# Optimization experiments

Hardware: AMD Instinct MI355X
Metric: run time of the kernel (lower is better)

## Reference

```python
import jax, jax.numpy as jnp
import numpy as np

TWO_PI = 2.0 * np.pi

def ringify(x):
    # wrap values to [-pi, pi)
    return (x + np.pi) % TWO_PI - np.pi

def complex_mean(x, axes):
    # circular mean direction: atan2(sum sin, sum ringify(cos))
    dir_x = ringify(jnp.cos(x)).sum(axis=axes)
    dir_y = jnp.sin(x).sum(axis=axes)
    return jnp.arctan2(dir_y, dir_x)

def setup_inputs() -> dict:
    key = jax.random.key(0)
    k1, k2, k3, k4 = jax.random.split(key, 4)
    B = 4096
    return {
        "x": jax.random.normal(k1, (B, 1, 28, 28), dtype=jnp.float32),
        "conv1_w": jax.random.normal(k2, (4, 1, 2, 2), dtype=jnp.float32),
        "conv2_w": jax.random.normal(k3, (8, 4, 4, 4), dtype=jnp.float32),
        "ff_w": jax.random.normal(k4, (288, 10), dtype=jnp.float32),
    }

def reference(x, conv1_w, conv2_w, ff_w):
    B = x.shape[0]
    x = ringify(x).reshape(B, 1, 28, 28)

    # --- ring conv1: 2x2 kernel, stride 2 (non-overlapping patches) ---
    # [B,1,28,28] -> [B,14,14,1,2,2]  (matches unfold(2,2,2).unfold(3,2,2).permute)
    p1 = x.reshape(B, 1, 14, 2, 14, 2).transpose(0, 2, 4, 1, 3, 5)
    w1 = conv1_w.transpose(1, 2, 3, 0)            # [1,2,2,4]
    d1 = ringify(p1[..., None] - w1)              # [B,14,14,1,2,2,4]
    h1 = complex_mean(d1, (3, 4, 5))              # [B,14,14,4]

    # --- ring conv2: 4x4 kernel, stride 2 (overlapping patches) ---
    h1 = h1.transpose(0, 3, 1, 2)                 # [B,4,14,14]
    idx = (jnp.arange(6) * 2)[:, None] + jnp.arange(4)[None, :]  # [6,4] window rows/cols
    p2 = h1[:, :, idx, :][:, :, :, :, idx]        # [B,4,6,4,6,4]
    p2 = p2.transpose(0, 2, 4, 1, 3, 5)           # [B,6,6,4,4,4]
    w2 = conv2_w.transpose(1, 2, 3, 0)            # [4,4,4,8]
    d2 = ringify(p2[..., None] - w2)              # [B,6,6,4,4,4,8]
    h2 = complex_mean(d2, (3, 4, 5))              # [B,6,6,8]

    # --- ring feed-forward ---
    f = h2.reshape(B, 288)
    d3 = ringify(f[:, :, None] - ff_w)            # [B,288,10]
    out = complex_mean(d3, (1,))                  # [B,10]
    return jnp.sin(out)
```

## Files before the change

### kernel.cpp

```cpp
#include <hip/hip_runtime.h>
#include <math.h>

#define W1_OFF 0
#define W2_OFF 16
#define NTRIG_SM 528
#define NFF 2880

__global__ void precompute_ff(const float* __restrict__ ff, float2* __restrict__ out) {
    int i = blockIdx.x * blockDim.x + threadIdx.x;
    if (i < NFF) {
        float s, c; sincosf(ff[i], &s, &c);
        out[i] = make_float2(c, s);
    }
}

template <bool USE_WS>
__global__ __launch_bounds__(640) void ringnn_kernel(
    const float* __restrict__ x,
    const float* __restrict__ w1g,
    const float* __restrict__ w2g,
    const float* __restrict__ ffg,
    const float2* __restrict__ fft_ws,
    float* __restrict__ out)
{
    __shared__ float2 trig[NTRIG_SM];
    __shared__ float2 sc1[2 * 784];
    __shared__ float2 sc2[2 * 288];
    __shared__ float2 ff_lds[USE_WS ? 1 : NFF];

    const int tid = threadIdx.x;

    if (tid < 16) {
        float s, c; __sincosf(w1g[tid], &s, &c);
        trig[W1_OFF + tid] = make_float2(c, s);
    }
    {
        int i = tid - 64;
        if (i >= 0 && i < 512) {
            int oc = i >> 6, e = i & 63;
            float s, c; __sincosf(w2g[i], &s, &c);
            trig[W2_OFF + e * 8 + oc] = make_float2(c, s);
        }
    }
    if (!USE_WS) {
        for (int i = tid; i < NFF; i += 640) {
            float s, c; __sincosf(ffg[i], &s, &c);
            ff_lds[i] = make_float2(c, s);
        }
    }
    __syncthreads();

    if (tid < 392) {
        int img = tid / 196, pos = tid % 196;
        int i = pos / 14, j = pos % 14;
        const float* xb = x + ((size_t)blockIdx.x * 2 + img) * 784;
        float2 r0 = *(const float2*)(xb + (2 * i) * 28 + 2 * j);
        float2 r1 = *(const float2*)(xb + (2 * i + 1) * 28 + 2 * j);
        float sx[4], cx[4];
        __sincosf(r0.x, &sx[0], &cx[0]);
        __sincosf(r0.y, &sx[1], &cx[1]);
        __sincosf(r1.x, &sx[2], &cx[2]);
        __sincosf(r1.y, &sx[3], &cx[3]);
        #pragma unroll
        for (int oc = 0; oc < 4; oc++) {
            float Y = 0.f, X = 0.f;
            #pragma unroll
            for (int e = 0; e < 4; e++) {
                float2 w = trig[W1_OFF + oc * 4 + e];
                Y = fmaf(sx[e], w.x, fmaf(-cx[e], w.y, Y));
                X = fmaf(cx[e], w.x, fmaf( sx[e], w.y, X));
            }
            float inv = rsqrtf(fmaxf(fmaf(X, X, Y * Y), 1e-30f));
            sc1[img * 784 + oc * 196 + pos] = make_float2(Y * inv, X * inv);
        }
    }
    __syncthreads();

    if (tid < 576) {
        int img = tid / 288;
        int r = tid % 288;
        int p = r >> 3, q = r & 7;
        int ocp = q >> 1, hf = q & 1;
        int oi = p / 6, oj = p % 6;
        const float2* scb = sc1 + img * 784;
        int base = oi * 28 + oj * 2;
        float Y0 = 0.f, X0 = 0.f, Y1 = 0.f, X1 = 0.f;
        #pragma unroll
        for (int ch = 0; ch < 4; ch++) {
            #pragma unroll
            for (int kk = 0; kk < 2; kk++) {
                int ki = hf * 2 + kk;
                #pragma unroll
                for (int jp = 0; jp < 2; jp++) {
                    int kj = jp * 2;
                    float4 sp = *(const float4*)(scb + ch * 196 + base + ki * 14 + kj);
                    int e = ch * 16 + ki * 4 + kj;
                    float4 w0 = *(const float4*)(&trig[W2_OFF + e * 8 + ocp * 2]);
                    float4 w1 = *(const float4*)(&trig[W2_OFF + (e + 1) * 8 + ocp * 2]);
                    Y0 = fmaf(sp.x, w0.x, fmaf(-sp.y, w0.y, Y0));
                    X0 = fmaf(sp.y, w0.x, fmaf( sp.x, w0.y, X0));
                    Y1 = fmaf(sp.x, w0.z, fmaf(-sp.y, w0.w, Y1));
                    X1 = fmaf(sp.y, w0.z, fmaf( sp.x, w0.w, X1));
                    Y0 = fmaf(sp.z, w1.x, fmaf(-sp.w, w1.y, Y0));
                    X0 = fmaf(sp.w, w1.x, fmaf( sp.z, w1.y, X0));
                    Y1 = fmaf(sp.z, w1.z, fmaf(-sp.w, w1.w, Y1));
                    X1 = fmaf(sp.w, w1.z, fmaf( sp.z, w1.w, X1));
                }
            }
        }
        Y0 += __shfl_xor(Y0, 1); X0 += __shfl_xor(X0, 1);
        Y1 += __shfl_xor(Y1, 1); X1 += __shfl_xor(X1, 1);
        float Y = hf ? Y1 : Y0;
        float X = hf ? X1 : X0;
        float inv = rsqrtf(fmaxf(fmaf(X, X, Y * Y), 1e-30f));
        sc2[img * 288 + p * 8 + ocp * 2 + hf] = make_float2(Y * inv, X * inv);
    }
    __syncthreads();

    {
        int img = tid / 320;
        int r = tid % 320;
        int n = r >> 5, s = r & 31;
        const float2* scb = sc2 + img * 288;
        float Y = 0.f, X = 0.f;
        #pragma unroll
        for (int i = 0; i < 9; i++) {
            int k = s * 9 + i;
            float2 sc = scb[k];
            float2 w;
            if (USE_WS) w = fft_ws[k * 10 + n];
            else        w = ff_lds[k * 10 + n];
            Y = fmaf(sc.x, w.x, fmaf(-sc.y, w.y, Y));
            X = fmaf(sc.y, w.x, fmaf( sc.x, w.y, X));
        }
        #pragma unroll
        for (int off = 16; off > 0; off >>= 1) {
            Y += __shfl_down(Y, off, 32);
            X += __shfl_down(X, off, 32);
        }
        if (s == 0) {
            size_t b = (size_t)blockIdx.x * 2 + img;
            out[b * 10 + n] = Y * rsqrtf(fmaxf(fmaf(X, X, Y * Y), 1e-30f));
        }
    }
}

extern "C" void kernel_launch(void* const* d_in, const int* in_sizes, int n_in,
                              void* d_out, int out_size, void* d_ws, size_t ws_size,
                              hipStream_t stream) {
    const float* x  = (const float*)d_in[0];
    const float* w1 = (const float*)d_in[1];
    const float* w2 = (const float*)d_in[2];
    const float* ff = (const float*)d_in[3];
    float* out = (float*)d_out;
    const int B = in_sizes[0] / 784;

    if (ws_size >= NFF * sizeof(float2)) {
        float2* fft = (float2*)d_ws;
        precompute_ff<<<(NFF + 255) / 256, 256, 0, stream>>>(ff, fft);
        ringnn_kernel<true><<<B / 2, 640, 0, stream>>>(x, w1, w2, ff, fft, out);
    } else {
        ringnn_kernel<false><<<B / 2, 640, 0, stream>>>(x, w1, w2, ff, nullptr, out);
    }
}
```

Baseline: 93.07 us.

## Drop ff precompute kernel, register-tile conv2, pad sc1 layout, recompute ff trig inline

Removes the separate ff precompute launch and workspace path. The feed-forward stage now computes sincos of the ff weights inline from global memory, with 16 lanes per output instead of 32. Conv2 is register-tiled so each thread computes three output columns and reuses loaded patches across kj, with only 192 threads active. The sc1 layout is padded to rows of 18, and the conv2 weights are regrouped per output-channel pair to allow wide LDS loads. This trades one fewer launch and less LDS traffic for redundant transcendental work in the FF stage and lower thread utilisation in conv2.

```diff
diff --git a/kernel.cpp b/kernel.cpp
--- a/kernel.cpp
+++ b/kernel.cpp
@@ -1,59 +1,36 @@
 #include <hip/hip_runtime.h>
 #include <math.h>
 
-#define W1_OFF 0
-#define W2_OFF 16
-#define NTRIG_SM 528
-#define NFF 2880
+#define B_PER_BLK 2
 
-__global__ void precompute_ff(const float* __restrict__ ff, float2* __restrict__ out) {
-    int i = blockIdx.x * blockDim.x + threadIdx.x;
-    if (i < NFF) {
-        float s, c; sincosf(ff[i], &s, &c);
-        out[i] = make_float2(c, s);
-    }
-}
-
-template <bool USE_WS>
 __global__ __launch_bounds__(640) void ringnn_kernel(
     const float* __restrict__ x,
     const float* __restrict__ w1g,
     const float* __restrict__ w2g,
     const float* __restrict__ ffg,
-    const float2* __restrict__ fft_ws,
     float* __restrict__ out)
 {
-    __shared__ float2 trig[NTRIG_SM];
-    __shared__ float2 sc1[2 * 784];
-    __shared__ float2 sc2[2 * 288];
-    __shared__ float2 ff_lds[USE_WS ? 1 : NFF];
-
+    __shared__ float2 trig1[16];
+    __shared__ float2 trig2[520];
+    __shared__ float2 sc1[B_PER_BLK * 1008];
+    __shared__ float2 sc2[B_PER_BLK * 288];
     const int tid = threadIdx.x;
 
     if (tid < 16) {
         float s, c; __sincosf(w1g[tid], &s, &c);
-        trig[W1_OFF + tid] = make_float2(c, s);
+        trig1[tid] = make_float2(c, s);
     }
-    {
-        int i = tid - 64;
-        if (i >= 0 && i < 512) {
-            int oc = i >> 6, e = i & 63;
-            float s, c; __sincosf(w2g[i], &s, &c);
-            trig[W2_OFF + e * 8 + oc] = make_float2(c, s);
-        }
-    }
-    if (!USE_WS) {
-        for (int i = tid; i < NFF; i += 640) {
-            float s, c; __sincosf(ffg[i], &s, &c);
-            ff_lds[i] = make_float2(c, s);
-        }
+    if (tid < 512) {
+        int oc = tid >> 6, e = tid & 63;
+        float s, c; __sincosf(w2g[tid], &s, &c);
+        trig2[(oc >> 1) * 130 + e * 2 + (oc & 1)] = make_float2(c, s);
     }
     __syncthreads();
 
     if (tid < 392) {
         int img = tid / 196, pos = tid % 196;
         int i = pos / 14, j = pos % 14;
-        const float* xb = x + ((size_t)blockIdx.x * 2 + img) * 784;
+        const float* xb = x + ((size_t)blockIdx.x * B_PER_BLK + img) * 784;
         float2 r0 = *(const float2*)(xb + (2 * i) * 28 + 2 * j);
         float2 r1 = *(const float2*)(xb + (2 * i + 1) * 28 + 2 * j);
         float sx[4], cx[4];
@@ -63,83 +40,93 @@
         __sincosf(r1.y, &sx[3], &cx[3]);
         #pragma unroll
         for (int oc = 0; oc < 4; oc++) {
+            float4 wa = *(const float4*)(&trig1[oc * 4]);
+            float4 wb = *(const float4*)(&trig1[oc * 4 + 2]);
             float Y = 0.f, X = 0.f;
-            #pragma unroll
-            for (int e = 0; e < 4; e++) {
-                float2 w = trig[W1_OFF + oc * 4 + e];
-                Y = fmaf(sx[e], w.x, fmaf(-cx[e], w.y, Y));
-                X = fmaf(cx[e], w.x, fmaf( sx[e], w.y, X));
-            }
+            Y = fmaf(sx[0], wa.x, fmaf(-cx[0], wa.y, Y));
+            X = fmaf(cx[0], wa.x, fmaf( sx[0], wa.y, X));
+            Y = fmaf(sx[1], wa.z, fmaf(-cx[1], wa.w, Y));
+            X = fmaf(cx[1], wa.z, fmaf( sx[1], wa.w, X));
+            Y = fmaf(sx[2], wb.x, fmaf(-cx[2], wb.y, Y));
+            X = fmaf(cx[2], wb.x, fmaf( sx[2], wb.y, X));
+            Y = fmaf(sx[3], wb.z, fmaf(-cx[3], wb.w, Y));
+            X = fmaf(cx[3], wb.z, fmaf( sx[3], wb.w, X));
             float inv = rsqrtf(fmaxf(fmaf(X, X, Y * Y), 1e-30f));
-            sc1[img * 784 + oc * 196 + pos] = make_float2(Y * inv, X * inv);
+            sc1[img * 1008 + oc * 252 + i * 18 + j] = make_float2(Y * inv, X * inv);
         }
     }
     __syncthreads();
 
-    if (tid < 576) {
-        int img = tid / 288;
-        int r = tid % 288;
-        int p = r >> 3, q = r & 7;
-        int ocp = q >> 1, hf = q & 1;
-        int oi = p / 6, oj = p % 6;
-        const float2* scb = sc1 + img * 784;
-        int base = oi * 28 + oj * 2;
-        float Y0 = 0.f, X0 = 0.f, Y1 = 0.f, X1 = 0.f;
+    if (tid < 192) {
+        int img = tid / 96, r = tid % 96;
+        int oi = r >> 4, ojg = (r >> 3) & 1, ocp = (r >> 1) & 3, hf = r & 1;
+        const float2* scb = sc1 + img * 1008;
+        const float2* wbp = trig2 + ocp * 130;
+        float aY[3][2] = {{0.f,0.f},{0.f,0.f},{0.f,0.f}};
+        float aX[3][2] = {{0.f,0.f},{0.f,0.f},{0.f,0.f}};
         #pragma unroll
         for (int ch = 0; ch < 4; ch++) {
             #pragma unroll
             for (int kk = 0; kk < 2; kk++) {
                 int ki = hf * 2 + kk;
+                int base = ch * 252 + (oi * 2 + ki) * 18 + ojg * 6;
+                float4 f0 = *(const float4*)(scb + base);
+                float4 f1 = *(const float4*)(scb + base + 2);
+                float4 f2 = *(const float4*)(scb + base + 4);
+                float4 f3 = *(const float4*)(scb + base + 6);
+                float ss[8] = {f0.x,f0.z,f1.x,f1.z,f2.x,f2.z,f3.x,f3.z};
+                float cc[8] = {f0.y,f0.w,f1.y,f1.w,f2.y,f2.w,f3.y,f3.w};
+                int e0 = ch * 16 + ki * 4;
                 #pragma unroll
-                for (int jp = 0; jp < 2; jp++) {
-                    int kj = jp * 2;
-                    float4 sp = *(const float4*)(scb + ch * 196 + base + ki * 14 + kj);
-                    int e = ch * 16 + ki * 4 + kj;
-                    float4 w0 = *(const float4*)(&trig[W2_OFF + e * 8 + ocp * 2]);
-                    float4 w1 = *(const float4*)(&trig[W2_OFF + (e + 1) * 8 + ocp * 2]);
-                    Y0 = fmaf(sp.x, w0.x, fmaf(-sp.y, w0.y, Y0));
-                    X0 = fmaf(sp.y, w0.x, fmaf( sp.x, w0.y, X0));
-                    Y1 = fmaf(sp.x, w0.z, fmaf(-sp.y, w0.w, Y1));
-                    X1 = fmaf(sp.y, w0.z, fmaf( sp.x, w0.w, X1));
-                    Y0 = fmaf(sp.z, w1.x, fmaf(-sp.w, w1.y, Y0));
-                    X0 = fmaf(sp.w, w1.x, fmaf( sp.z, w1.y, X0));
-                    Y1 = fmaf(sp.z, w1.z, fmaf(-sp.w, w1.w, Y1));
-                    X1 = fmaf(sp.w, w1.z, fmaf( sp.z, w1.w, X1));
+                for (int kj = 0; kj < 4; kj++) {
+                    float4 wv = *(const float4*)(wbp + (e0 + kj) * 2);
+                    #pragma unroll
+                    for (int ojl = 0; ojl < 3; ojl++) {
+                        float s = ss[ojl * 2 + kj], c = cc[ojl * 2 + kj];
+                        aY[ojl][0] = fmaf(s, wv.x, fmaf(-c, wv.y, aY[ojl][0]));
+                        aX[ojl][0] = fmaf(c, wv.x, fmaf( s, wv.y, aX[ojl][0]));
+                        aY[ojl][1] = fmaf(s, wv.z, fmaf(-c, wv.w, aY[ojl][1]));
+                        aX[ojl][1] = fmaf(c, wv.z, fmaf( s, wv.w, aX[ojl][1]));
+                    }
                 }
             }
         }
-        Y0 += __shfl_xor(Y0, 1); X0 += __shfl_xor(X0, 1);
-        Y1 += __shfl_xor(Y1, 1); X1 += __shfl_xor(X1, 1);
-        float Y = hf ? Y1 : Y0;
-        float X = hf ? X1 : X0;
-        float inv = rsqrtf(fmaxf(fmaf(X, X, Y * Y), 1e-30f));
-        sc2[img * 288 + p * 8 + ocp * 2 + hf] = make_float2(Y * inv, X * inv);
+        #pragma unroll
+        for (int ojl = 0; ojl < 3; ojl++) {
+            float y0 = aY[ojl][0]; y0 += __shfl_xor(y0, 1);
+            float y1 = aY[ojl][1]; y1 += __shfl_xor(y1, 1);
+            float x0 = aX[ojl][0]; x0 += __shfl_xor(x0, 1);
+            float x1 = aX[ojl][1]; x1 += __shfl_xor(x1, 1);
+            float Y = hf ? y1 : y0;
+            float X = hf ? x1 : x0;
+            float inv = rsqrtf(fmaxf(fmaf(X, X, Y * Y), 1e-30f));
+            int p = oi * 6 + ojg * 3 + ojl;
+            sc2[img * 288 + p * 8 + ocp * 2 + hf] = make_float2(Y * inv, X * inv);
+        }
     }
     __syncthreads();
 
-    {
-        int img = tid / 320;
-        int r = tid % 320;
-        int n = r >> 5, s = r & 31;
+    if (tid < 320) {
+        int img = tid / 160, r = tid % 160;
+        int n = r >> 4, s = r & 15;
         const float2* scb = sc2 + img * 288;
         float Y = 0.f, X = 0.f;
         #pragma unroll
-        for (int i = 0; i < 9; i++) {
-            int k = s * 9 + i;
+        for (int i = 0; i < 18; i++) {
+            int k = s * 18 + i;
             float2 sc = scb[k];
-            float2 w;
-            if (USE_WS) w = fft_ws[k * 10 + n];
-            else        w = ff_lds[k * 10 + n];
-            Y = fmaf(sc.x, w.x, fmaf(-sc.y, w.y, Y));
-            X = fmaf(sc.y, w.x, fmaf( sc.x, w.y, X));
+            float ws_, wc_;
+            __sincosf(ffg[k * 10 + n], &ws_, &wc_);
+            Y = fmaf(sc.x, wc_, fmaf(-sc.y, ws_, Y));
+            X = fmaf(sc.y, wc_, fmaf( sc.x, ws_, X));
         }
         #pragma unroll
-        for (int off = 16; off > 0; off >>= 1) {
-            Y += __shfl_down(Y, off, 32);
-            X += __shfl_down(X, off, 32);
+        for (int off = 1; off < 16; off <<= 1) {
+            Y += __shfl_xor(Y, off);
+            X += __shfl_xor(X, off);
         }
         if (s == 0) {
-            size_t b = (size_t)blockIdx.x * 2 + img;
+            size_t b = (size_t)blockIdx.x * B_PER_BLK + img;
             out[b * 10 + n] = Y * rsqrtf(fmaxf(fmaf(X, X, Y * Y), 1e-30f));
         }
     }
@@ -154,12 +141,5 @@
     const float* ff = (const float*)d_in[3];
     float* out = (float*)d_out;
     const int B = in_sizes[0] / 784;
-
-    if (ws_size >= NFF * sizeof(float2)) {
-        float2* fft = (float2*)d_ws;
-        precompute_ff<<<(NFF + 255) / 256, 256, 0, stream>>>(ff, fft);
-        ringnn_kernel<true><<<B / 2, 640, 0, stream>>>(x, w1, w2, ff, fft, out);
-    } else {
-        ringnn_kernel<false><<<B / 2, 640, 0, stream>>>(x, w1, w2, ff, nullptr, out);
-    }
+    ringnn_kernel<<<B / B_PER_BLK, 640, 0, stream>>>(x, w1, w2, ff, out);
 }
```

Result: faster. 91.13 us (-2.1%).
